# Kernel optimization log

Measured on AMD Instinct MI355X. Metric: run time of the kernel, lower is better.

## Reference

```python
import jax, jax.numpy as jnp
import numpy as np

B, T, H = 4, 2048, 1024
NH = 16
HD = H // NH  # 64
NEG_INF = -1.0e9  # module uses -1e9, not -inf


def setup_inputs() -> dict:
    key = jax.random.key(0)
    k1, k2, k3 = jax.random.split(key, 3)
    x = jax.random.normal(k1, (B, T, H), dtype=jnp.float32)
    W_qkv = jax.random.normal(k2, (3 * H, H), dtype=jnp.float32) * (1.0 / np.sqrt(H))
    W_out = jax.random.normal(k3, (H, H), dtype=jnp.float32) * (1.0 / np.sqrt(H))
    return {"x": x, "W_qkv": W_qkv, "W_out": W_out}


def reference(x, W_qkv, W_out):
    Bx, Tx, C = x.shape
    qkv = x @ W_qkv.T                              # [B,T,3H]
    q, k, v = jnp.split(qkv, 3, axis=-1)
    # [B,T,H] -> [B,NH,T,HD]
    q = q.reshape(Bx, Tx, NH, HD).transpose(0, 2, 1, 3)
    k = k.reshape(Bx, Tx, NH, HD).transpose(0, 2, 1, 3)
    v = v.reshape(Bx, Tx, NH, HD).transpose(0, 2, 1, 3)
    scale = 1.0 / np.sqrt(HD)
    scores = jnp.einsum('bhqd,bhkd->bhqk', q, k) * scale  # [B,NH,T,T]
    causal = jnp.tril(jnp.ones((Tx, Tx), dtype=bool))[None, None]
    scores = jnp.where(causal, scores, jnp.asarray(NEG_INF, scores.dtype))
    attn = jax.nn.softmax(scores, axis=-1)
    out = jnp.einsum('bhqk,bhkd->bhqd', attn, v)   # [B,NH,T,HD]
    out = out.transpose(0, 2, 1, 3).reshape(Bx, Tx, C)
    return out @ W_out.T
```

## Files before the change

### kernel.cpp

```cpp
#include <hip/hip_runtime.h>
#include <hip/hip_bf16.h>


typedef unsigned short ushort_t;
typedef __attribute__((ext_vector_type(8))) short  s8v;
typedef __attribute__((ext_vector_type(4))) float  f4v;
typedef __attribute__((ext_vector_type(4))) unsigned int u4v;

__device__ inline ushort_t f2bf(float f) {
    unsigned u = __builtin_bit_cast(unsigned, f);
    u += 0x7fffu + ((u >> 16) & 1u);
    return (ushort_t)(u >> 16);
}

__device__ inline void gload16(const ushort_t* g, ushort_t* l) {
    __builtin_amdgcn_global_load_lds(
        (const __attribute__((address_space(1))) unsigned int*)g,
        (__attribute__((address_space(3))) unsigned int*)l, 16, 0, 0);
}

__global__ __launch_bounds__(256) void cast_all(
    const float* __restrict__ x, const float* __restrict__ wqkv,
    const float* __restrict__ wout, ushort_t* __restrict__ xb,
    ushort_t* __restrict__ wqkvb, ushort_t* __restrict__ woutb)
{
    int i = blockIdx.x * 256 + threadIdx.x;
    const float* src; ushort_t* dst; int off;
    if (i < 1048576)      { src = x;    dst = xb;    off = i; }
    else if (i < 1441792) { src = wqkv; dst = wqkvb; off = i - 1048576; }
    else                  { src = wout; dst = woutb; off = i - 1441792; }
    const float* p = src + (size_t)off * 8;
    f4v a = *(const f4v*)p;
    f4v b = *(const f4v*)(p + 4);
    union { u4v v; ushort_t u[8]; } o;
    #pragma unroll
    for (int j = 0; j < 4; j++) { o.u[j] = f2bf(a[j]); o.u[j + 4] = f2bf(b[j]); }
    *(u4v*)(dst + (size_t)off * 8) = o.v;
}

template<int MODE>
__global__ __launch_bounds__(256) void gemm_nt(
    const ushort_t* __restrict__ A, const ushort_t* __restrict__ Bm,
    ushort_t* __restrict__ o0, ushort_t* __restrict__ o1, ushort_t* __restrict__ o2,
    float* __restrict__ of)
{
    __shared__ __align__(16) ushort_t SH[16384];

    const int tid  = threadIdx.x;
    const int m0   = blockIdx.x * 128;
    const int n0   = blockIdx.y * 128;
    const int wave = tid >> 6, lane = tid & 63;
    const int wr = wave >> 1, wc = wave & 1;
    const int lhi = lane >> 4, llo = lane & 15;
    const int srow = lane >> 2;
    const int scol = (((lane & 3) ^ ((srow >> 1) & 3)) * 8);

    auto stage = [&](int k0, int buf) {
        #pragma unroll
        for (int p = 0; p < 2; p++) {
            int chunk = wave * 2 + p;
            int row = chunk * 16 + srow;
            gload16(A  + (size_t)(m0 + row) * 1024 + k0 + scol,
                    &SH[buf * 4096 + chunk * 512 + lane * 8]);
            gload16(Bm + (size_t)(n0 + row) * 1024 + k0 + scol,
                    &SH[8192 + buf * 4096 + chunk * 512 + lane * 8]);
        }
    };

    f4v acc[4][4] = {};
    int buf = 0;

    stage(0, 0);
    __syncthreads();

    for (int k0 = 0; k0 < 1024; k0 += 32) {
        if (k0 + 32 < 1024) stage(k0 + 32, buf ^ 1);

        const int rch = (lhi ^ ((llo >> 1) & 3)) * 8;
        s8v a[4], b[4];
        #pragma unroll
        for (int i = 0; i < 4; i++)
            a[i] = *(const s8v*)&SH[buf * 4096 + (wr * 64 + i * 16 + llo) * 32 + rch];
        #pragma unroll
        for (int i = 0; i < 4; i++)
            b[i] = *(const s8v*)&SH[8192 + buf * 4096 + (wc * 64 + i * 16 + llo) * 32 + rch];
        #pragma unroll
        for (int i = 0; i < 4; i++)
            #pragma unroll
            for (int j = 0; j < 4; j++)
                acc[i][j] = __builtin_amdgcn_mfma_f32_16x16x32_bf16(a[i], b[j], acc[i][j], 0, 0, 0);

        __syncthreads();
        buf ^= 1;
    }

    if (MODE == 0 && n0 >= 2048) {
        const int hbase = (n0 - 2048) >> 6;
        const int t0b   = m0 & 2047;
        const int bb    = m0 >> 11;
        #pragma unroll 1
        for (int p = 0; p < 2; p++) {
            __syncthreads();
            if (wr == p) {
                #pragma unroll
                for (int i = 0; i < 4; i++)
                    #pragma unroll
                    for (int j = 0; j < 4; j++) {
                        union { unsigned long long q; ushort_t u[4]; } w;
                        #pragma unroll
                        for (int r = 0; r < 4; r++) w.u[r] = f2bf(acc[i][j][r]);
                        int nrel = wc * 64 + j * 16 + llo;
                        *(unsigned long long*)&SH[nrel * 68 + i * 16 + lhi * 4] = w.q;
                    }
            }
            __syncthreads();
            #pragma unroll
            for (int cc = 0; cc < 4; cc++) {
                int c  = cc * 256 + tid;
                int nn = c >> 3, sp0 = (c & 7) * 8;
                union { s8v v; ushort_t u[8]; } o;
                #pragma unroll
                for (int i2 = 0; i2 < 8; i2++) {
                    int sp = sp0 + i2;
                    int k  = ((sp >> 5) << 5) | ((sp & 1) << 4) | ((sp & 31) >> 1);
                    o.u[i2] = SH[nn * 68 + k];
                }
                int head = hbase + (nn >> 6), d = nn & 63;
                size_t bh = (size_t)(bb * 16 + head);
                *(s8v*)(o2 + ((bh * 64 + d) * 2048 + t0b + p * 64 + sp0)) = o.v;
            }
        }
        return;
    }

    #pragma unroll
    for (int i = 0; i < 4; i++) {
        #pragma unroll
        for (int j = 0; j < 4; j++) {
            #pragma unroll
            for (int r = 0; r < 4; r++) {
                int m = m0 + wr * 64 + i * 16 + lhi * 4 + r;
                int n = n0 + wc * 64 + j * 16 + llo;
                if (MODE == 1) {
                    of[(size_t)m * 1024 + n] = acc[i][j][r];
                } else {
                    float val = acc[i][j][r];
                    int b  = m >> 11, t = m & 2047;
                    int which = n >> 10, hh = n & 1023;
                    int head = hh >> 6, d = hh & 63;
                    size_t bh = (size_t)(b * 16 + head);
                    if (which == 0)
                        o0[(size_t)m * 1024 + hh] = f2bf(val * 0.18033688011112042f);
                    else
                        o1[(bh * 2048 + t) * 64 + d] = f2bf(val);
                }
            }
        }
    }
}

__global__ __launch_bounds__(512, 4) void attn_kernel(
    const ushort_t* __restrict__ q_ws, const ushort_t* __restrict__ k_ws,
    const ushort_t* __restrict__ v_ws, ushort_t* __restrict__ ao_ws)
{
    const int p    = blockIdx.x;
    const int bh   = blockIdx.y;
    const int tid  = threadIdx.x;
    const int wave = tid >> 6, lane = tid & 63;
    const int lhi = lane >> 4, llo = lane & 15;
    const int b = bh >> 4, head = bh & 15;

    const ushort_t* Kb = k_ws + (size_t)bh * 2048 * 64;
    const ushort_t* Vb = v_ws + (size_t)bh * 64 * 2048;

    __shared__ __align__(16) ushort_t Ks [2][4096];
    __shared__ __align__(16) ushort_t Vts[2][4096];
    __shared__ __align__(16) ushort_t Ps [8][2][1280];

    const int srow = wave * 8 + (lane >> 3);
    const int gch  = ((lane & 7) ^ (srow & 7)) * 8;
    auto stage = [&](int t, int buf) {
        const int kk0 = t * 64;
        gload16(Kb + (size_t)(kk0 + srow) * 64 + gch,
                &Ks[buf][srow * 64 + (lane & 7) * 8]);
        gload16(Vb + (size_t)srow * 2048 + kk0 + gch,
                &Vts[buf][srow * 64 + (lane & 7) * 8]);
    };

    const int qt  = (wave >> 2) ? (15 - p) : p;
    const int wq0 = qt * 128 + (wave & 3) * 32;

    s8v qf[2][2];
    #pragma unroll
    for (int g = 0; g < 2; g++) {
        const ushort_t* Qp = q_ws + (size_t)(b * 2048 + wq0 + g * 16 + llo) * 1024 + head * 64;
        qf[g][0] = *(const s8v*)(Qp + lhi * 8);
        qf[g][1] = *(const s8v*)(Qp + 32 + lhi * 8);
    }

    f4v o[2][4] = {};
    float lsum[2][4] = {};

    const int ntb = 32 - 2 * p;
    const int xs  = llo & 7;
    int cur = 0;

    stage(0, 0);
    __syncthreads();

    #pragma unroll 1
    for (int t = 0; t < ntb; t++) {
        if (t + 1 < ntb) stage(t + 1, cur ^ 1);

        const int kk0 = t * 64;
        if (kk0 <= wq0 + 31) {
            f4v s0[4], s1[4];
            #pragma unroll
            for (int c = 0; c < 4; c++) {
                const int rb = (c * 16 + llo) * 64;
                s8v kb0 = *(const s8v*)&Ks[cur][rb + ((lhi    ) ^ xs) * 8];
                s8v kb1 = *(const s8v*)&Ks[cur][rb + ((4 + lhi) ^ xs) * 8];
                f4v z0 = {}, z1 = {};
                z0 = __builtin_amdgcn_mfma_f32_16x16x32_bf16(qf[0][0], kb0, z0, 0, 0, 0);
                z0 = __builtin_amdgcn_mfma_f32_16x16x32_bf16(qf[0][1], kb1, z0, 0, 0, 0);
                z1 = __builtin_amdgcn_mfma_f32_16x16x32_bf16(qf[1][0], kb0, z1, 0, 0, 0);
                z1 = __builtin_amdgcn_mfma_f32_16x16x32_bf16(qf[1][1], kb1, z1, 0, 0, 0);
                s0[c] = z0; s1[c] = z1;
            }

            #pragma unroll
            for (int g = 0; g < 2; g++) {
                const int qrb = wq0 + g * 16;
                f4v* s = g ? s1 : s0;
                if ((kk0 + 63) > qrb) {
                    #pragma unroll
                    for (int c = 0; c < 4; c++) {
                        int kkg = kk0 + c * 16 + llo;
                        #pragma unroll
                        for (int r = 0; r < 4; r++)
                            if (kkg > qrb + lhi * 4 + r) s[c][r] = -1e9f;
                    }
                }
                #pragma unroll
                for (int h = 0; h < 2; h++) {
                    #pragma unroll
                    for (int r = 0; r < 4; r++) {
                        float p0 = __builtin_amdgcn_exp2f(s[2 * h][r]);
                        float p1 = __builtin_amdgcn_exp2f(s[2 * h + 1][r]);
                        lsum[g][r] += p0 + p1;
                        unsigned pk;
                        asm("v_cvt_pk_bf16_f32 %0, %1, %2" : "=v"(pk) : "v"(p0), "v"(p1));
                        *(unsigned*)&Ps[wave][g][h * 640 + (lhi * 4 + r) * 40 + llo * 2] = pk;
                    }
                }
            }

            s8v pa[2][2];
            #pragma unroll
            for (int g = 0; g < 2; g++) {
                pa[g][0] = *(const s8v*)&Ps[wave][g][llo * 40 + lhi * 8];
                pa[g][1] = *(const s8v*)&Ps[wave][g][640 + llo * 40 + lhi * 8];
            }
            #pragma unroll
            for (int cd = 0; cd < 4; cd++) {
                const int rb = (cd * 16 + llo) * 64;
                s8v vb0 = *(const s8v*)&Vts[cur][rb + ((lhi    ) ^ xs) * 8];
                s8v vb1 = *(const s8v*)&Vts[cur][rb + ((4 + lhi) ^ xs) * 8];
                #pragma unroll
                for (int g = 0; g < 2; g++) {
                    o[g][cd] = __builtin_amdgcn_mfma_f32_16x16x32_bf16(pa[g][0], vb0, o[g][cd], 0, 0, 0);
                    o[g][cd] = __builtin_amdgcn_mfma_f32_16x16x32_bf16(pa[g][1], vb1, o[g][cd], 0, 0, 0);
                }
            }
        }

        __syncthreads();
        cur ^= 1;
    }

    #pragma unroll
    for (int off = 1; off < 16; off <<= 1)
        #pragma unroll
        for (int g = 0; g < 2; g++)
            #pragma unroll
            for (int r = 0; r < 4; r++)
                lsum[g][r] += __shfl_xor(lsum[g][r], off, 64);

    #pragma unroll
    for (int g = 0; g < 2; g++)
        #pragma unroll
        for (int cd = 0; cd < 4; cd++)
            #pragma unroll
            for (int r = 0; r < 4; r++) {
                int qq = wq0 + g * 16 + lhi * 4 + r;
                int d  = cd * 16 + llo;
                ao_ws[((size_t)(b * 2048 + qq)) * 1024 + head * 64 + d] =
                    f2bf(o[g][cd][r] / lsum[g][r]);
            }
}

extern "C" void kernel_launch(void* const* d_in, const int* in_sizes, int n_in,
                              void* d_out, int out_size, void* d_ws, size_t ws_size,
                              hipStream_t stream) {
    const float* x    = (const float*)d_in[0];
    const float* wqkv = (const float*)d_in[1];
    const float* wout = (const float*)d_in[2];

    ushort_t* wqkvb = (ushort_t*)d_ws;
    ushort_t* woutb = wqkvb + 3145728;
    ushort_t* xb    = woutb + 1048576;
    ushort_t* q_ws  = xb + 8388608;
    ushort_t* k_ws  = q_ws + 8388608;
    ushort_t* v_ws  = k_ws + 8388608;
    ushort_t* ao_ws = xb;
    float*    out   = (float*)d_out;

    cast_all<<<6144, 256, 0, stream>>>(x, wqkv, wout, xb, wqkvb, woutb);
    gemm_nt<0><<<dim3(64, 24), 256, 0, stream>>>(xb, wqkvb, q_ws, k_ws, v_ws, nullptr);
    attn_kernel<<<dim3(8, 64), 512, 0, stream>>>(q_ws, k_ws, v_ws, ao_ws);
    gemm_nt<1><<<dim3(64, 8), 256, 0, stream>>>(ao_ws, woutb, nullptr, nullptr, nullptr, out);
}
```

Measured before the change: 228.7 us.

## Deepen GEMM K-tile to 64, reorder attention blocks, add MFMA priority hints

```diff
diff --git a/kernel.cpp b/kernel.cpp
--- a/kernel.cpp
+++ b/kernel.cpp
@@ -44,7 +44,7 @@
     ushort_t* __restrict__ o0, ushort_t* __restrict__ o1, ushort_t* __restrict__ o2,
     float* __restrict__ of)
 {
-    __shared__ __align__(16) ushort_t SH[16384];
+    __shared__ __align__(16) ushort_t SH[32768];
 
     const int tid  = threadIdx.x;
     const int m0   = blockIdx.x * 128;
@@ -52,43 +52,46 @@
     const int wave = tid >> 6, lane = tid & 63;
     const int wr = wave >> 1, wc = wave & 1;
     const int lhi = lane >> 4, llo = lane & 15;
-    const int srow = lane >> 2;
-    const int scol = (((lane & 3) ^ ((srow >> 1) & 3)) * 8);
+    const int sgch = ((lane & 7) ^ (lane >> 3)) * 8;
 
     auto stage = [&](int k0, int buf) {
         #pragma unroll
-        for (int p = 0; p < 2; p++) {
-            int chunk = wave * 2 + p;
-            int row = chunk * 16 + srow;
-            gload16(A  + (size_t)(m0 + row) * 1024 + k0 + scol,
-                    &SH[buf * 4096 + chunk * 512 + lane * 8]);
-            gload16(Bm + (size_t)(n0 + row) * 1024 + k0 + scol,
-                    &SH[8192 + buf * 4096 + chunk * 512 + lane * 8]);
+        for (int p = 0; p < 4; p++) {
+            int row = wave * 32 + p * 8 + (lane >> 3);
+            gload16(A  + (size_t)(m0 + row) * 1024 + k0 + sgch,
+                    &SH[buf * 8192 + row * 64 + (lane & 7) * 8]);
+            gload16(Bm + (size_t)(n0 + row) * 1024 + k0 + sgch,
+                    &SH[16384 + buf * 8192 + row * 64 + (lane & 7) * 8]);
         }
     };
 
     f4v acc[4][4] = {};
     int buf = 0;
+    const int xs = llo & 7;
 
     stage(0, 0);
     __syncthreads();
 
-    for (int k0 = 0; k0 < 1024; k0 += 32) {
-        if (k0 + 32 < 1024) stage(k0 + 32, buf ^ 1);
-
-        const int rch = (lhi ^ ((llo >> 1) & 3)) * 8;
-        s8v a[4], b[4];
-        #pragma unroll
-        for (int i = 0; i < 4; i++)
-            a[i] = *(const s8v*)&SH[buf * 4096 + (wr * 64 + i * 16 + llo) * 32 + rch];
-        #pragma unroll
-        for (int i = 0; i < 4; i++)
-            b[i] = *(const s8v*)&SH[8192 + buf * 4096 + (wc * 64 + i * 16 + llo) * 32 + rch];
-        #pragma unroll
-        for (int i = 0; i < 4; i++)
-            #pragma unroll
-            for (int j = 0; j < 4; j++)
-                acc[i][j] = __builtin_amdgcn_mfma_f32_16x16x32_bf16(a[i], b[j], acc[i][j], 0, 0, 0);
+    for (int k0 = 0; k0 < 1024; k0 += 64) {
+        if (k0 + 64 < 1024) stage(k0 + 64, buf ^ 1);
+
+        #pragma unroll
+        for (int s = 0; s < 2; s++) {
+            s8v a[4], b[4];
+            #pragma unroll
+            for (int i = 0; i < 4; i++)
+                a[i] = *(const s8v*)&SH[buf * 8192
+                        + (wr * 64 + i * 16 + llo) * 64 + ((s * 4 + lhi) ^ xs) * 8];
+            #pragma unroll
+            for (int i = 0; i < 4; i++)
+                b[i] = *(const s8v*)&SH[16384 + buf * 8192
+                        + (wc * 64 + i * 16 + llo) * 64 + ((s * 4 + lhi) ^ xs) * 8];
+            #pragma unroll
+            for (int i = 0; i < 4; i++)
+                #pragma unroll
+                for (int j = 0; j < 4; j++)
+                    acc[i][j] = __builtin_amdgcn_mfma_f32_16x16x32_bf16(a[i], b[j], acc[i][j], 0, 0, 0);
+        }
 
         __syncthreads();
         buf ^= 1;
@@ -163,8 +166,8 @@
     const ushort_t* __restrict__ q_ws, const ushort_t* __restrict__ k_ws,
     const ushort_t* __restrict__ v_ws, ushort_t* __restrict__ ao_ws)
 {
-    const int p    = blockIdx.x;
     const int bh   = blockIdx.y;
+    const int p    = (bh < 32) ? blockIdx.x : 7 - blockIdx.x;
     const int tid  = threadIdx.x;
     const int wave = tid >> 6, lane = tid & 63;
     const int lhi = lane >> 4, llo = lane & 15;
@@ -215,6 +218,7 @@
         const int kk0 = t * 64;
         if (kk0 <= wq0 + 31) {
             f4v s0[4], s1[4];
+            __builtin_amdgcn_s_setprio(1);
             #pragma unroll
             for (int c = 0; c < 4; c++) {
                 const int rb = (c * 16 + llo) * 64;
@@ -227,6 +231,7 @@
                 z1 = __builtin_amdgcn_mfma_f32_16x16x32_bf16(qf[1][1], kb1, z1, 0, 0, 0);
                 s0[c] = z0; s1[c] = z1;
             }
+            __builtin_amdgcn_s_setprio(0);
 
             #pragma unroll
             for (int g = 0; g < 2; g++) {
@@ -261,6 +266,7 @@
                 pa[g][0] = *(const s8v*)&Ps[wave][g][llo * 40 + lhi * 8];
                 pa[g][1] = *(const s8v*)&Ps[wave][g][640 + llo * 40 + lhi * 8];
             }
+            __builtin_amdgcn_s_setprio(1);
             #pragma unroll
             for (int cd = 0; cd < 4; cd++) {
                 const int rb = (cd * 16 + llo) * 64;
@@ -272,6 +278,7 @@
                     o[g][cd] = __builtin_amdgcn_mfma_f32_16x16x32_bf16(pa[g][1], vb1, o[g][cd], 0, 0, 0);
                 }
             }
+            __builtin_amdgcn_s_setprio(0);
         }
 
         __syncthreads();
```

Result: no change. 225.5 us (-1.4%).
